# Performance work log

Measured on AMD Instinct MI355X. Metric: run time of the kernel, lower is better.

## Reference

```python
import jax, jax.numpy as jnp
import numpy as np

NUM_NEG = 100            # number of negative samples per masked step
CLAMP_W = 1.0            # clamped_logit_weight
B, C, T, M = 8, 256, 1024, 512


def setup_inputs() -> dict:
    key = jax.random.key(0)
    k1, k2, k3 = jax.random.split(key, 3)
    feat_proj = jax.random.normal(k1, (B, C, T), dtype=jnp.float32)
    context_output = jax.random.normal(k2, (B, C, T), dtype=jnp.float32)
    # exactly M masked timesteps per batch row (random positions)
    perm = jax.vmap(lambda k: jax.random.permutation(k, T))(jax.random.split(k3, B))
    mask = perm < M  # [B, T] bool, M True per row
    return {"feat_proj": feat_proj, "mask": mask,
            "context_output": context_output, "num_masked": M}


def reference(feat_proj, mask, context_output, num_masked):
    Bb, Cc, Tt = feat_proj.shape
    # indices of masked timesteps, in time order (stable argsort) -> [B, M]
    idx = jnp.argsort(jnp.logical_not(mask), axis=1)[:, :num_masked]
    feat_t = jnp.swapaxes(feat_proj, 1, 2)        # [B, T, C]
    ctx_t = jnp.swapaxes(context_output, 1, 2)    # [B, T, C]
    mf = jnp.take_along_axis(feat_t, idx[:, :, None], axis=1)  # [B, M, C]
    mc = jnp.take_along_axis(ctx_t, idx[:, :, None], axis=1)   # [B, M, C]
    # uniform sampling of NUM_NEG negatives without replacement, excluding self:
    # random scores per (t, candidate), self set to -1, take top-k
    scores = jax.random.uniform(jax.random.key(42), (Bb, num_masked, num_masked))
    self_mask = jnp.eye(num_masked, dtype=bool)
    scores = jnp.where(self_mask[None], -1.0, scores)
    _, neg_idx = jax.lax.top_k(scores, NUM_NEG)                 # [B, M, K]
    neg_feats = jnp.take_along_axis(mf[:, None, :, :], neg_idx[..., None], axis=2)  # [B, M, K, C]
    pos_logit = jnp.einsum('bmc,bmc->bm', mc, mf)               # [B, M]
    neg_logit = jnp.einsum('bmc,bmkc->bmk', mc, neg_feats)      # [B, M, K]
    logits = jnp.concatenate([pos_logit[..., None], neg_logit], axis=-1)  # [B, M, 1+K]
    total_loss = jnp.sum(jax.nn.softmax(logits, axis=-1)[..., 0])
    clamped = CLAMP_W * jnp.tanh(logits / CLAMP_W)
    total_aux_loss = jnp.sum(clamped ** 2)
    return total_loss, total_aux_loss
```

## Files before the change

### kernel.cpp

```cpp
#include <hip/hip_runtime.h>
#include <stdint.h>

#define NB   8
#define NC   256
#define NT   1024
#define NM   512
#define NNEG 100

__device__ __forceinline__ unsigned rotl32(unsigned x, int d) {
  return (x << d) | (x >> (32 - d));
}

__device__ unsigned threefry_bits(unsigned i) {
  const unsigned half = 1048576u;
  const bool lo = i < half;
  unsigned v0 = lo ? i : (i - half);
  unsigned v1 = lo ? (i + half) : i;
  const unsigned k0 = 0u, k1 = 42u;
  const unsigned k2 = k0 ^ k1 ^ 0x1BD11BDAu;
  v0 += k0; v1 += k1;
#define TF_R(r) { v0 += v1; v1 = rotl32(v1, r); v1 ^= v0; }
  TF_R(13) TF_R(15) TF_R(26) TF_R(6)
  v0 += k1; v1 += k2 + 1u;
  TF_R(17) TF_R(29) TF_R(16) TF_R(24)
  v0 += k2; v1 += k0 + 2u;
  TF_R(13) TF_R(15) TF_R(26) TF_R(6)
  v0 += k0; v1 += k1 + 3u;
  TF_R(17) TF_R(29) TF_R(16) TF_R(24)
  v0 += k1; v1 += k2 + 4u;
  TF_R(13) TF_R(15) TF_R(26) TF_R(6)
  v0 += k2; v1 += k0 + 5u;
#undef TF_R
  return lo ? v0 : v1;
}

__global__ __launch_bounds__(1024) void k_idx(const void* __restrict__ maskp,
                                              int* __restrict__ idxp) {
  __shared__ int sc[1024];
  __shared__ int sflag;
  const int t = threadIdx.x;
  const int b = blockIdx.x;
  const unsigned char* mb = (const unsigned char*)maskp;

  int c1 = (mb[t] != 0) ? 1 : 0;
  int c4 = (((const unsigned*)mb)[t] != 0u) ? 1 : 0;
  int c8 = (((const unsigned long long*)mb)[t] != 0ull) ? 1 : 0;
  sc[t] = c1 + (c4 << 11) + (c8 << 22);
  __syncthreads();
  for (int off = 512; off > 0; off >>= 1) {
    if (t < off) sc[t] += sc[t + off];
    __syncthreads();
  }
  if (t == 0) {
    int c1s = sc[0] & 2047, c4s = (sc[0] >> 11) & 2047, c8s = (sc[0] >> 22) & 2047;
    sflag = (c4s == 512) ? 4 : ((c1s == 512) ? 1 : ((c8s == 512) ? 8 : 4));
  }
  __syncthreads();
  const int stride = sflag;

  const size_t e = (size_t)b * NT + t;
  int f;
  if (stride == 1)      f = (mb[e] != 0);
  else if (stride == 4) f = (((const unsigned*)mb)[e] != 0u);
  else                  f = (((const unsigned long long*)mb)[e] != 0ull);

  __syncthreads();
  sc[t] = f;
  __syncthreads();
  for (int off = 1; off < 1024; off <<= 1) {
    int v = sc[t];
    int add = (t >= off) ? sc[t - off] : 0;
    __syncthreads();
    sc[t] = v + add;
    __syncthreads();
  }
  if (f) idxp[b * NM + (sc[t] - 1)] = t;
}

__global__ __launch_bounds__(256) void k_gemm(const float* __restrict__ ctx,
                                              const float* __restrict__ feat,
                                              const int* __restrict__ idxp,
                                              float* __restrict__ S) {
  __shared__ float At[16][68];
  __shared__ float Bt[16][68];
  __shared__ int tA[64], tB[64];

  const int tid = threadIdx.x;
  const int b  = blockIdx.z;
  const int m0 = blockIdx.y * 64;
  const int j0 = blockIdx.x * 64;

  if (tid < 64)       tA[tid]      = idxp[b * NM + m0 + tid];
  else if (tid < 128) tB[tid - 64] = idxp[b * NM + j0 + (tid - 64)];
  __syncthreads();

  const float* cb = ctx  + (size_t)b * NC * NT;
  const float* fb = feat + (size_t)b * NC * NT;

  float acc[4][4];
#pragma unroll
  for (int i = 0; i < 4; ++i)
#pragma unroll
    for (int k = 0; k < 4; ++k) acc[i][k] = 0.f;

  const int ty = tid >> 4, tx = tid & 15;

  for (int c0 = 0; c0 < NC; c0 += 16) {
#pragma unroll
    for (int p = 0; p < 4; ++p) {
      int ee = tid + p * 256;
      int mm = ee & 63;
      int cc = ee >> 6;
      At[cc][mm] = cb[(size_t)(c0 + cc) * NT + tA[mm]];
      Bt[cc][mm] = fb[(size_t)(c0 + cc) * NT + tB[mm]];
    }
    __syncthreads();
#pragma unroll
    for (int cc = 0; cc < 16; ++cc) {
      float a0 = At[cc][ty * 4 + 0], a1 = At[cc][ty * 4 + 1];
      float a2 = At[cc][ty * 4 + 2], a3 = At[cc][ty * 4 + 3];
      float b0 = Bt[cc][tx * 4 + 0], b1 = Bt[cc][tx * 4 + 1];
      float b2 = Bt[cc][tx * 4 + 2], b3 = Bt[cc][tx * 4 + 3];
      acc[0][0] += a0 * b0; acc[0][1] += a0 * b1; acc[0][2] += a0 * b2; acc[0][3] += a0 * b3;
      acc[1][0] += a1 * b0; acc[1][1] += a1 * b1; acc[1][2] += a1 * b2; acc[1][3] += a1 * b3;
      acc[2][0] += a2 * b0; acc[2][1] += a2 * b1; acc[2][2] += a2 * b2; acc[2][3] += a2 * b3;
      acc[3][0] += a3 * b0; acc[3][1] += a3 * b1; acc[3][2] += a3 * b2; acc[3][3] += a3 * b3;
    }
    __syncthreads();
  }

#pragma unroll
  for (int i = 0; i < 4; ++i) {
    float4 v = make_float4(acc[i][0], acc[i][1], acc[i][2], acc[i][3]);
    *(float4*)&S[((size_t)b * NM + m0 + ty * 4 + i) * NM + j0 + tx * 4] = v;
  }
}

__global__ __launch_bounds__(512) void k_loss(const float* __restrict__ S,
                                              float* __restrict__ pl,
                                              float* __restrict__ pa) {
  __shared__ unsigned hist[256];
  __shared__ unsigned long long bkey[512];
  __shared__ int bcount;
  __shared__ int boundary_bin, need_s;
  __shared__ unsigned char selflag[512];
  __shared__ float redM[8], redE[8], redA[8];
  __shared__ float posnum;

  const int t = threadIdx.x;
  const int row = blockIdx.x;
  const int m = row & (NM - 1);
  const bool self = (t == m);

  unsigned bits = threefry_bits((unsigned)row * 512u + (unsigned)t);
  unsigned u = bits >> 9;
  unsigned key = (u << 9) | (unsigned)(511 - t);
  int bin = (int)(u >> 15);

  if (t < 256) hist[t] = 0;
  if (t == 0) bcount = 0;
  selflag[t] = 0;
  __syncthreads();

  if (!self) atomicAdd(&hist[bin], 1u);
  __syncthreads();

  if (t < 64) {
    unsigned h0 = hist[4 * t + 0], h1 = hist[4 * t + 1];
    unsigned h2 = hist[4 * t + 2], h3 = hist[4 * t + 3];
    unsigned s = h0 + h1 + h2 + h3;
    unsigned suf = s;
#pragma unroll
    for (int off = 1; off < 64; off <<= 1) {
      unsigned o = __shfl_down(suf, off, 64);
      if (t + off < 64) suf += o;
    }
    unsigned a3 = suf - s;
    unsigned a2 = a3 + h3;
    unsigned a1 = a2 + h2;
    unsigned a0 = a1 + h1;
    if (a3 < NNEG && a3 + h3 >= NNEG) { boundary_bin = 4 * t + 3; need_s = NNEG - (int)a3; }
    if (a2 < NNEG && a2 + h2 >= NNEG) { boundary_bin = 4 * t + 2; need_s = NNEG - (int)a2; }
    if (a1 < NNEG && a1 + h1 >= NNEG) { boundary_bin = 4 * t + 1; need_s = NNEG - (int)a1; }
    if (a0 < NNEG && a0 + h0 >= NNEG) { boundary_bin = 4 * t + 0; need_s = NNEG - (int)a0; }
  }
  __syncthreads();

  const int bb = boundary_bin;
  if (!self) {
    if (bin > bb) selflag[t] = 1;
    else if (bin == bb) {
      int p = atomicAdd(&bcount, 1);
      bkey[p] = (((unsigned long long)key) << 1) | 1ull;
    }
  }
  __syncthreads();

  if (t == 0) {
    int cnt = bcount, need = need_s;
    for (int it = 0; it < need; ++it) {
      unsigned long long best = 0ull; int bi = 0;
      for (int q = 0; q < cnt; ++q)
        if (bkey[q] > best) { best = bkey[q]; bi = q; }
      bkey[bi] = 0ull;
      int tt = 511 - (int)((best >> 1) & 511ull);
      selflag[tt] = 1;
    }
  }
  __syncthreads();

  const float* Srow = S + (size_t)row * NM;
  const bool act = (selflag[t] != 0) || self;
  const float logitv = Srow[t];
  const int wid = t >> 6;

  float mv = act ? logitv : -3.4e38f;
#pragma unroll
  for (int off = 32; off > 0; off >>= 1) mv = fmaxf(mv, __shfl_xor(mv, off, 64));
  if ((t & 63) == 0) redM[wid] = mv;
  __syncthreads();
  float mx = redM[0];
#pragma unroll
  for (int q = 1; q < 8; ++q) mx = fmaxf(mx, redM[q]);

  float e = 0.f, a = 0.f;
  if (act) {
    e = expf(logitv - mx);
    float th = tanhf(logitv);
    a = th * th;
  }
  if (self) posnum = e;

  float es = e, as = a;
#pragma unroll
  for (int off = 32; off > 0; off >>= 1) {
    es += __shfl_xor(es, off, 64);
    as += __shfl_xor(as, off, 64);
  }
  if ((t & 63) == 0) { redE[wid] = es; redA[wid] = as; }
  __syncthreads();

  if (t == 0) {
    float den = 0.f, aux = 0.f;
#pragma unroll
    for (int q = 0; q < 8; ++q) { den += redE[q]; aux += redA[q]; }
    pl[row] = posnum / den;
    pa[row] = aux;
  }
}

__global__ __launch_bounds__(1024) void k_red(const float* __restrict__ pl,
                                              const float* __restrict__ pa,
                                              float* __restrict__ out) {
  __shared__ float s1[1024], s2[1024];
  const int t = threadIdx.x;
  float a = 0.f, b = 0.f;
  for (int q = t; q < NB * NM; q += 1024) { a += pl[q]; b += pa[q]; }
  s1[t] = a; s2[t] = b;
  __syncthreads();
  for (int off = 512; off > 0; off >>= 1) {
    if (t < off) { s1[t] += s1[t + off]; s2[t] += s2[t + off]; }
    __syncthreads();
  }
  if (t == 0) { out[0] = s1[0]; out[1] = s2[0]; }
}

extern "C" void kernel_launch(void* const* d_in, const int* in_sizes, int n_in,
                              void* d_out, int out_size, void* d_ws, size_t ws_size,
                              hipStream_t stream) {
  const float* feat = (const float*)d_in[0];
  const void*  mask = d_in[1];
  const float* ctx  = (const float*)d_in[2];
  float* out = (float*)d_out;

  char* ws = (char*)d_ws;
  int*   idxp = (int*)ws;
  float* S    = (float*)(ws + 16384);
  float* pl   = (float*)(ws + 16384 + (size_t)NB * NM * NM * 4);
  float* pa   = pl + NB * NM;

  k_idx<<<NB, 1024, 0, stream>>>(mask, idxp);

  dim3 g2(NM / 64, NM / 64, NB);
  k_gemm<<<g2, 256, 0, stream>>>(ctx, feat, idxp, S);

  k_loss<<<NB * NM, 512, 0, stream>>>(S, pl, pa);

  k_red<<<1, 1024, 0, stream>>>(pl, pa, out);
}
```

Measured before the change: 56.15 us.

## Compact masked columns into contiguous matrices before GEMM, use wave-level scan

Adds a compaction kernel that gathers the masked timesteps of ctx and feat, through shared memory, into contiguous [B,M,C] matrices. The GEMM can then load float4 rows with register prefetch instead of doing strided gathers with uncoalesced 4-byte reads. The index kernel becomes a single block of 8 waves that uses shuffle-based prefix scans and also emits a position map. The loss kernel switches to fast __expf and an exp-based tanh, trading a little accuracy. The cost is an extra kernel launch and an extra write and read pass over the compacted data.

```diff
diff --git a/kernel.cpp b/kernel.cpp
--- a/kernel.cpp
+++ b/kernel.cpp
@@ -34,68 +34,104 @@
   return lo ? v0 : v1;
 }
 
-__global__ __launch_bounds__(1024) void k_idx(const void* __restrict__ maskp,
-                                              int* __restrict__ idxp) {
-  __shared__ int sc[1024];
+__global__ __launch_bounds__(512) void k_idx(const void* __restrict__ maskp,
+                                             int* __restrict__ idxp,
+                                             int* __restrict__ pos) {
   __shared__ int sflag;
   const int t = threadIdx.x;
-  const int b = blockIdx.x;
+  const int lane = t & 63, w = t >> 6;
   const unsigned char* mb = (const unsigned char*)maskp;
 
-  int c1 = (mb[t] != 0) ? 1 : 0;
-  int c4 = (((const unsigned*)mb)[t] != 0u) ? 1 : 0;
-  int c8 = (((const unsigned long long*)mb)[t] != 0ull) ? 1 : 0;
-  sc[t] = c1 + (c4 << 11) + (c8 << 22);
-  __syncthreads();
-  for (int off = 512; off > 0; off >>= 1) {
-    if (t < off) sc[t] += sc[t + off];
-    __syncthreads();
-  }
-  if (t == 0) {
-    int c1s = sc[0] & 2047, c4s = (sc[0] >> 11) & 2047, c8s = (sc[0] >> 22) & 2047;
-    sflag = (c4s == 512) ? 4 : ((c1s == 512) ? 1 : ((c8s == 512) ? 8 : 4));
+  if (w == 0) {
+    int c1 = 0, c4 = 0, c8 = 0;
+    for (int j = 0; j < 16; ++j) {
+      int p = lane * 16 + j;
+      c1 += (mb[p] != 0);
+      c4 += (((const unsigned*)mb)[p] != 0u);
+      c8 += (((const unsigned long long*)mb)[p] != 0ull);
+    }
+#pragma unroll
+    for (int off = 32; off > 0; off >>= 1) {
+      c1 += __shfl_xor(c1, off, 64);
+      c4 += __shfl_xor(c4, off, 64);
+      c8 += __shfl_xor(c8, off, 64);
+    }
+    if (lane == 0) sflag = (c4 == 512) ? 4 : ((c1 == 512) ? 1 : ((c8 == 512) ? 8 : 4));
   }
   __syncthreads();
   const int stride = sflag;
-
-  const size_t e = (size_t)b * NT + t;
-  int f;
-  if (stride == 1)      f = (mb[e] != 0);
-  else if (stride == 4) f = (((const unsigned*)mb)[e] != 0u);
-  else                  f = (((const unsigned long long*)mb)[e] != 0ull);
-
-  __syncthreads();
-  sc[t] = f;
-  __syncthreads();
-  for (int off = 1; off < 1024; off <<= 1) {
-    int v = sc[t];
-    int add = (t >= off) ? sc[t - off] : 0;
-    __syncthreads();
-    sc[t] = v + add;
-    __syncthreads();
-  }
-  if (f) idxp[b * NM + (sc[t] - 1)] = t;
-}
-
-__global__ __launch_bounds__(256) void k_gemm(const float* __restrict__ ctx,
-                                              const float* __restrict__ feat,
-                                              const int* __restrict__ idxp,
-                                              float* __restrict__ S) {
+  const int b = w;
+
+  unsigned fm = 0; int cnt = 0;
+  for (int j = 0; j < 16; ++j) {
+    int tt = lane * 16 + j;
+    size_t e = (size_t)b * NT + tt;
+    int f;
+    if (stride == 1)      f = (mb[e] != 0);
+    else if (stride == 4) f = (((const unsigned*)mb)[e] != 0u);
+    else                  f = (((const unsigned long long*)mb)[e] != 0ull);
+    fm |= ((unsigned)f) << j;
+    cnt += f;
+  }
+  int pre = cnt;
+#pragma unroll
+  for (int off = 1; off < 64; off <<= 1) {
+    int o = __shfl_up(pre, off, 64);
+    if (lane >= off) pre += o;
+  }
+  int base = pre - cnt;
+  for (int j = 0; j < 16; ++j) {
+    int tt = lane * 16 + j;
+    int masked = (fm >> j) & 1;
+    pos[b * NT + tt] = masked ? base : -1;
+    if (masked) { idxp[b * NM + base] = tt; base++; }
+  }
+}
+
+__global__ __launch_bounds__(256) void k_compact(const float* __restrict__ ctx,
+                                                 const float* __restrict__ feat,
+                                                 const int* __restrict__ pos,
+                                                 float* __restrict__ MC,
+                                                 float* __restrict__ MF) {
+  __shared__ float lds[64][129];
+  const int tid = threadIdx.x;
+  const int t0 = blockIdx.x * 128;
+  const int c0 = blockIdx.y * 64;
+  const int b = blockIdx.z >> 1, mat = blockIdx.z & 1;
+  const float* src = (mat ? feat : ctx) + (size_t)b * NC * NT;
+  float* dst = (mat ? MF : MC) + (size_t)b * NM * NC;
+
+  const int c4 = tid >> 6;
+  const int tl = tid & 63;
+  for (int ci = 0; ci < 16; ++ci) {
+    int cc = c4 * 16 + ci;
+#pragma unroll
+    for (int tj = 0; tj < 2; ++tj) {
+      int tt = tl + 64 * tj;
+      lds[cc][tt] = src[(size_t)(c0 + cc) * NT + t0 + tt];
+    }
+  }
+  __syncthreads();
+
+  const int* posb = pos + b * NT + t0;
+  const int tr = tid >> 6;
+  for (int tt = tr; tt < 128; tt += 4) {
+    int p = posb[tt];
+    if (p >= 0) dst[(size_t)p * NC + c0 + tl] = lds[tl][tt];
+  }
+}
+
+__global__ __launch_bounds__(256) void k_gemm2(const float* __restrict__ MC,
+                                               const float* __restrict__ MF,
+                                               float* __restrict__ S) {
   __shared__ float At[16][68];
   __shared__ float Bt[16][68];
-  __shared__ int tA[64], tB[64];
-
   const int tid = threadIdx.x;
-  const int b  = blockIdx.z;
-  const int m0 = blockIdx.y * 64;
-  const int j0 = blockIdx.x * 64;
-
-  if (tid < 64)       tA[tid]      = idxp[b * NM + m0 + tid];
-  else if (tid < 128) tB[tid - 64] = idxp[b * NM + j0 + (tid - 64)];
-  __syncthreads();
-
-  const float* cb = ctx  + (size_t)b * NC * NT;
-  const float* fb = feat + (size_t)b * NC * NT;
+  const int b = blockIdx.z, m0 = blockIdx.y * 64, j0 = blockIdx.x * 64;
+  const float* Ab = MC + ((size_t)b * NM + m0) * NC;
+  const float* Bb = MF + ((size_t)b * NM + j0) * NC;
+  const int row = tid >> 2, q = tid & 3;
+  const int ty = tid >> 4, tx = tid & 15;
 
   float acc[4][4];
 #pragma unroll
@@ -103,18 +139,19 @@
 #pragma unroll
     for (int k = 0; k < 4; ++k) acc[i][k] = 0.f;
 
-  const int ty = tid >> 4, tx = tid & 15;
+  float4 av = *(const float4*)(Ab + (size_t)row * NC + 4 * q);
+  float4 bv = *(const float4*)(Bb + (size_t)row * NC + 4 * q);
 
   for (int c0 = 0; c0 < NC; c0 += 16) {
-#pragma unroll
-    for (int p = 0; p < 4; ++p) {
-      int ee = tid + p * 256;
-      int mm = ee & 63;
-      int cc = ee >> 6;
-      At[cc][mm] = cb[(size_t)(c0 + cc) * NT + tA[mm]];
-      Bt[cc][mm] = fb[(size_t)(c0 + cc) * NT + tB[mm]];
-    }
+    At[4 * q + 0][row] = av.x; At[4 * q + 1][row] = av.y;
+    At[4 * q + 2][row] = av.z; At[4 * q + 3][row] = av.w;
+    Bt[4 * q + 0][row] = bv.x; Bt[4 * q + 1][row] = bv.y;
+    Bt[4 * q + 2][row] = bv.z; Bt[4 * q + 3][row] = bv.w;
     __syncthreads();
+    if (c0 + 16 < NC) {
+      av = *(const float4*)(Ab + (size_t)row * NC + c0 + 16 + 4 * q);
+      bv = *(const float4*)(Bb + (size_t)row * NC + c0 + 16 + 4 * q);
+    }
 #pragma unroll
     for (int cc = 0; cc < 16; ++cc) {
       float a0 = At[cc][ty * 4 + 0], a1 = At[cc][ty * 4 + 1];
@@ -225,8 +262,8 @@
 
   float e = 0.f, a = 0.f;
   if (act) {
-    e = expf(logitv - mx);
-    float th = tanhf(logitv);
+    e = __expf(logitv - mx);
+    float th = 1.f - 2.f / (__expf(2.f * logitv) + 1.f);
     a = th * th;
   }
   if (self) posnum = e;
@@ -275,14 +312,21 @@
 
   char* ws = (char*)d_ws;
   int*   idxp = (int*)ws;
-  float* S    = (float*)(ws + 16384);
-  float* pl   = (float*)(ws + 16384 + (size_t)NB * NM * NM * 4);
-  float* pa   = pl + NB * NM;
-
-  k_idx<<<NB, 1024, 0, stream>>>(mask, idxp);
+  int*   pos  = (int*)(ws + 16384);
+  char*  base = ws + 65536;
+  float* MC = (float*)base;
+  float* MF = (float*)(base + (4u << 20));
+  float* S  = (float*)(base + (8u << 20));
+  float* pl = (float*)(base + (16u << 20));
+  float* pa = pl + NB * NM;
+
+  k_idx<<<1, 512, 0, stream>>>(mask, idxp, pos);
+
+  dim3 gc(NT / 128, NC / 64, NB * 2);
+  k_compact<<<gc, 256, 0, stream>>>(ctx, feat, pos, MC, MF);
 
   dim3 g2(NM / 64, NM / 64, NB);
-  k_gemm<<<g2, 256, 0, stream>>>(ctx, feat, idxp, S);
+  k_gemm2<<<g2, 256, 0, stream>>>(MC, MF, S);
 
   k_loss<<<NB * NM, 512, 0, stream>>>(S, pl, pa);
 
```

Result: slower. 67.97 us (+21.0%).
